# Performance work log

Hardware: AMD Instinct MI355X
Metric: run time of the kernel (lower is better)

Reference implementation:

```python
import jax, jax.numpy as jnp
import numpy as np

KV_POOL = 2


def setup_inputs() -> dict:
    key = jax.random.key(0)
    ks = jax.random.split(key, 12)
    B, C1, C2, H, W, D = 8, 256, 512, 64, 64, 64
    s = 0.02
    return {
        "x1": jax.random.normal(ks[0], (B, C1, H, W), jnp.float32),
        "x2": jax.random.normal(ks[1], (B, C2, H, W), jnp.float32),
        "Wq": jax.random.normal(ks[2], (D, C1), jnp.float32) * s,
        "bq": jnp.zeros((D,), jnp.float32),
        "Wk": jax.random.normal(ks[3], (D, C2), jnp.float32) * s,
        "bk": jnp.zeros((D,), jnp.float32),
        "Wv": jax.random.normal(ks[4], (D, C2), jnp.float32) * s,
        "bv": jnp.zeros((D,), jnp.float32),
        "Wo": jax.random.normal(ks[5], (C1, D), jnp.float32) * s,
        "bo": jnp.zeros((C1,), jnp.float32),
    }


def reference(x1, x2, Wq, bq, Wk, bk, Wv, bv, Wo, bo):
    B, C1, H, W = x1.shape
    D = Wq.shape[0]
    # adaptive_avg_pool2d to (H//2, W//2) with even dims == 2x2 mean pool
    Bs, C2, H2, W2 = x2.shape
    x2p = x2.reshape(Bs, C2, H2 // KV_POOL, KV_POOL, W2 // KV_POOL, KV_POOL).mean(axis=(3, 5))
    # 1x1 convs as channel matmuls; flatten spatial dims
    Q = jnp.einsum('bchw,dc->bhwd', x1, Wq).reshape(B, H * W, D) + bq          # [B,N,D]
    K = jnp.einsum('bchw,dc->bhwd', x2p, Wk).reshape(B, -1, D) + bk            # [B,M,D]
    V = jnp.einsum('bchw,dc->bhwd', x2p, Wv).reshape(B, -1, D) + bv            # [B,M,D]
    attn = jax.nn.softmax(jnp.einsum('bnd,bmd->bnm', Q, K), axis=-1)           # [B,N,M]
    out = jnp.einsum('bnm,bmd->bnd', attn, V)                                  # [B,N,D]
    y = jnp.einsum('bnd,cd->bnc', out, Wo) + bo                                # [B,N,C1]
    y = y.reshape(B, H, W, C1).transpose(0, 3, 1, 2)                           # [B,C1,H,W]
    return x1 + y
```

## Files before the change

### kernel.cpp

```cpp
#include <hip/hip_runtime.h>
#include <hip/hip_bf16.h>

typedef __bf16 bf16x4 __attribute__((ext_vector_type(4)));
typedef __bf16 bf16x8 __attribute__((ext_vector_type(8)));
typedef float f32x16 __attribute__((ext_vector_type(16)));
typedef unsigned int u32x4 __attribute__((ext_vector_type(4)));

static constexpr int Bc = 8, C1 = 256, C2 = 512, Hh = 64, Ww = 64, Dd = 64;
static constexpr int Nn = 4096, Mm = 1024;

#define MFMA __builtin_amdgcn_mfma_f32_32x32x16_bf16

__device__ __forceinline__ uint32_t pkbf(float a, float b) {
  union { __bf16 h[2]; uint32_t u; } x;
  x.h[0] = (__bf16)a; x.h[1] = (__bf16)b;
  return x.u;
}

__device__ __forceinline__ bf16x8 cvt8(const float* __restrict__ p) {
  float4 a = *(const float4*)p;
  float4 b2 = *(const float4*)(p + 4);
  bf16x8 r;
  r[0] = (__bf16)a.x; r[1] = (__bf16)a.y; r[2] = (__bf16)a.z; r[3] = (__bf16)a.w;
  r[4] = (__bf16)b2.x; r[5] = (__bf16)b2.y; r[6] = (__bf16)b2.z; r[7] = (__bf16)b2.w;
  return r;
}

__device__ __forceinline__ void pack16(const float* p, bf16x8& f0, bf16x8& f1) {
  uint32_t w01 = pkbf(p[0], p[1]),   w23 = pkbf(p[2], p[3]);
  uint32_t w45 = pkbf(p[4], p[5]),   w67 = pkbf(p[6], p[7]);
  uint32_t w89 = pkbf(p[8], p[9]),   wab = pkbf(p[10], p[11]);
  uint32_t wcd = pkbf(p[12], p[13]), wef = pkbf(p[14], p[15]);
  auto s0 = __builtin_amdgcn_permlane32_swap(w01, w45, false, false);
  auto s1 = __builtin_amdgcn_permlane32_swap(w23, w67, false, false);
  auto s2 = __builtin_amdgcn_permlane32_swap(w89, wcd, false, false);
  auto s3 = __builtin_amdgcn_permlane32_swap(wab, wef, false, false);
  u32x4 q0 = {s0[0], s1[0], s0[1], s1[1]};
  u32x4 q1 = {s2[0], s3[0], s2[1], s3[1]};
  f0 = __builtin_bit_cast(bf16x8, q0);
  f1 = __builtin_bit_cast(bf16x8, q1);
}


__global__ __launch_bounds__(256) void k_stage(
    const float* __restrict__ x1, const float* __restrict__ x2,
    const float* __restrict__ Wq, const float* __restrict__ Wk,
    const float* __restrict__ Wv, const float* __restrict__ Wo,
    __bf16* __restrict__ wqf, __bf16* __restrict__ wkf,
    __bf16* __restrict__ wvf, __bf16* __restrict__ wof,
    __bf16* __restrict__ x1f, __bf16* __restrict__ x2pf) {
  __shared__ __align__(16) __bf16 lds[32 * 132];
  const int lin = blockIdx.x, tid = threadIdx.x;
  if (lin >= 4096) {
    int t = (lin - 4096) * 256 + tid;
    if (t < 2048) {
      int l = t & 63, g = t >> 6, dh = g >> 4, ks = g & 15;
      int d = dh * 32 + (l & 31), c = ks * 16 + (l >> 5) * 8;
      *(bf16x8*)(wqf + (size_t)t * 8) = cvt8(Wq + (size_t)d * C1 + c);
    } else if (t < 6144) {
      int tt = t - 2048;
      int l = tt & 63, g = tt >> 6, dh = g >> 5, ks = g & 31;
      int d = dh * 32 + (l & 31), c = ks * 16 + (l >> 5) * 8;
      *(bf16x8*)(wkf + (size_t)tt * 8) = cvt8(Wk + (size_t)d * C2 + c);
    } else if (t < 10240) {
      int tt = t - 6144;
      int l = tt & 63, g = tt >> 6, dh = g >> 5, ks = g & 31;
      int d = dh * 32 + (l & 31), c = ks * 16 + (l >> 5) * 8;
      *(bf16x8*)(wvf + (size_t)tt * 8) = cvt8(Wv + (size_t)d * C2 + c);
    } else if (t < 12288) {
      int tt = t - 10240;
      int l = tt & 63, g = tt >> 6, ct = g >> 2, ks = g & 3;
      int crow = ct * 32 + (l & 31), d = ks * 16 + (l >> 5) * 8;
      *(bf16x8*)(wof + (size_t)tt * 8) = cvt8(Wo + (size_t)crow * Dd + d);
    }
    return;
  }
  const int b = lin & 7, idx = lin >> 3;
  const int w = tid >> 6, l = tid & 63;

  if (idx < 256) {
    const int t = idx >> 1, cc = idx & 1;
    const int n0 = t * 32, c0 = cc * 128;
#pragma unroll
    for (int it = 0; it < 4; ++it) {
      int cl = it * 32 + (tid >> 3);
      int q = tid & 7;
      float4 v = *(const float4*)(x1 + (size_t)(b * C1 + c0 + cl) * Nn + n0 + 4 * q);
      lds[(4 * q + 0) * 132 + cl] = (__bf16)v.x;
      lds[(4 * q + 1) * 132 + cl] = (__bf16)v.y;
      lds[(4 * q + 2) * 132 + cl] = (__bf16)v.z;
      lds[(4 * q + 3) * 132 + cl] = (__bf16)v.w;
    }
    __syncthreads();
#pragma unroll
    for (int j = 0; j < 2; ++j) {
      int ks8 = w * 2 + j;
      int off = (l & 31) * 132 + ks8 * 16 + (l >> 5) * 8;
      bf16x4 lo = *(const bf16x4*)(lds + off);
      bf16x4 hi = *(const bf16x4*)(lds + off + 4);
      __bf16* dst = x1f + ((size_t)(b * 128 + t) * 16 + cc * 8 + ks8) * 512 + l * 8;
      *(bf16x4*)dst = lo;
      *(bf16x4*)(dst + 4) = hi;
    }
  } else {
    const int idx2 = idx - 256;
    const int t = idx2 >> 3, cc = idx2 & 7;
    const int c0 = cc * 64;
    const int g = tid >> 4, lane16 = tid & 15, row = g & 1;
#pragma unroll
    for (int it = 0; it < 8; ++it) {
      int cl = it * 8 + (g >> 1);
      const float* p =
          x2 + ((size_t)(b * C2 + c0 + cl) * Hh + 2 * t + row) * Ww + 4 * lane16;
      float4 v = *(const float4*)p;
      float s0 = v.x + v.y, s1 = v.z + v.w;
      float p0 = (s0 + __shfl_xor(s0, 16)) * 0.25f;
      float p1 = (s1 + __shfl_xor(s1, 16)) * 0.25f;
      if (row == 0) {
        lds[(2 * lane16) * 68 + cl] = (__bf16)p0;
        lds[(2 * lane16 + 1) * 68 + cl] = (__bf16)p1;
      }
    }
    __syncthreads();
    const int ks8 = w;
    int off = (l & 31) * 68 + ks8 * 16 + (l >> 5) * 8;
    bf16x4 lo = *(const bf16x4*)(lds + off);
    bf16x4 hi = *(const bf16x4*)(lds + off + 4);
    __bf16* dst = x2pf + ((size_t)(b * 32 + t) * 32 + cc * 4 + ks8) * 512 + l * 8;
    *(bf16x4*)dst = lo;
    *(bf16x4*)(dst + 4) = hi;
  }
}

__global__ __launch_bounds__(256) void k_proj(
    const __bf16* __restrict__ x1f, const __bf16* __restrict__ x2pf,
    const __bf16* __restrict__ wqf, const float* __restrict__ bq,
    const __bf16* __restrict__ wkf, const float* __restrict__ bk,
    const __bf16* __restrict__ wvf, const float* __restrict__ bv,
    __bf16* __restrict__ qfb, __bf16* __restrict__ kfb,
    __bf16* __restrict__ vfb) {
  const int lin = blockIdx.x;
  const int b = lin & 7, idx = lin >> 3;
  const int tid = threadIdx.x;
  const int w = tid >> 6, l = tid & 63, h = l >> 5, nl = l & 31;

  if (idx < 64) {
    const int nsub = w & 1, dh = w >> 1;
    const int t = idx * 2 + nsub;
    const __bf16* af = x1f + ((size_t)(b * 128 + t) * 16) * 512 + l * 8;
    const __bf16* wf = wqf + (size_t)dh * 16 * 512 + l * 8;
    f32x16 acc = {};
#pragma unroll
    for (int ks = 0; ks < 16; ++ks) {
      bf16x8 a = *(const bf16x8*)(af + ks * 512);
      bf16x8 bb = *(const bf16x8*)(wf + ks * 512);
      acc = MFMA(a, bb, acc, 0, 0, 0);
    }
    const int d = dh * 32 + nl;
    const float bias = bq[d];
    __bf16* qdst = qfb + (size_t)b * Nn * Dd + (size_t)t * 2048 +
                   (d >> 4) * 512 + ((d >> 3) & 1) * 256 + (d & 7);
#pragma unroll
    for (int r = 0; r < 16; ++r) {
      int mrow = (r & 3) + 8 * (r >> 2) + 4 * h;
      qdst[mrow * 8] = (__bf16)(acc[r] + bias);
    }
  } else {
    const int h2 = idx - 64;
    const int isv = w >> 1, dh = w & 1;
    const __bf16* af = x2pf + ((size_t)(b * 32 + h2) * 32) * 512 + l * 8;
    const __bf16* wf = (isv ? wvf : wkf) + (size_t)dh * 32 * 512 + l * 8;
    f32x16 acc = {};
#pragma unroll
    for (int ks = 0; ks < 32; ++ks) {
      bf16x8 a = *(const bf16x8*)(af + ks * 512);
      bf16x8 bb = *(const bf16x8*)(wf + ks * 512);
      acc = MFMA(a, bb, acc, 0, 0, 0);
    }
    const int d = dh * 32 + nl;
    if (!isv) {
      const float bias = bk[d];
      __bf16* kdst = kfb + (size_t)b * Mm * Dd + (size_t)h2 * 2048 +
                     (d >> 4) * 512 + ((d >> 3) & 1) * 256 + (d & 7);
#pragma unroll
      for (int r = 0; r < 16; ++r) {
        int mr = (r & 3) + 8 * (r >> 2) + 4 * h;
        kdst[mr * 8] = (__bf16)(acc[r] + bias);
      }
    } else {
      const float bias = bv[d];
      float ov[16];
#pragma unroll
      for (int r = 0; r < 16; ++r) ov[r] = acc[r] + bias;
      bf16x8 f0, f1;
      pack16(ov, f0, f1);
      __bf16* vdst = vfb + (size_t)b * Mm * Dd + (size_t)h2 * 2048 + l * 8;
      *(bf16x8*)(vdst + (size_t)dh * 512) = f0;
      *(bf16x8*)(vdst + (size_t)(2 + dh) * 512) = f1;
    }
  }
}

template <int S>
__global__ __launch_bounds__(256) void k_attn_part(
    const __bf16* __restrict__ qfb, const __bf16* __restrict__ kfb,
    const __bf16* __restrict__ vfb, __bf16* __restrict__ po,
    float* __restrict__ pml) {
  const int lin = blockIdx.x;
  const int b = lin & 7, rest = lin >> 3, nblk = rest & 31, sp = rest >> 5;
  const int tid = threadIdx.x;
  const int w = tid >> 6, l = tid & 63, h = l >> 5, nl = l & 31;
  const int n = nblk * 128 + w * 32 + nl;
  constexpr int NT = Mm / S / 32;
  const int t0 = sp * NT;

  const __bf16* qt = qfb + (size_t)b * Nn * Dd + (size_t)(nblk * 4 + w) * 2048 + l * 8;
  bf16x8 qf0 = *(const bf16x8*)(qt);
  bf16x8 qf1 = *(const bf16x8*)(qt + 512);
  bf16x8 qf2 = *(const bf16x8*)(qt + 1024);
  bf16x8 qf3 = *(const bf16x8*)(qt + 1536);

  const __bf16* kt = kfb + (size_t)b * Mm * Dd + (size_t)t0 * 2048 + l * 8;
  const __bf16* vt = vfb + (size_t)b * Mm * Dd + (size_t)t0 * 2048 + l * 8;

  f32x16 o0 = {}, o1 = {};
  float lsum = 0.f;

  bf16x8 ck0 = *(const bf16x8*)(kt);
  bf16x8 ck1 = *(const bf16x8*)(kt + 512);
  bf16x8 ck2 = *(const bf16x8*)(kt + 1024);
  bf16x8 ck3 = *(const bf16x8*)(kt + 1536);
  bf16x8 cv0 = *(const bf16x8*)(vt);
  bf16x8 cv1 = *(const bf16x8*)(vt + 512);
  bf16x8 cv2 = *(const bf16x8*)(vt + 1024);
  bf16x8 cv3 = *(const bf16x8*)(vt + 1536);

#pragma unroll
  for (int i = 0; i < NT; ++i) {
    bf16x8 nk0, nk1, nk2, nk3, nv0, nv1, nv2, nv3;
    if (i + 1 < NT) {
      const __bf16* kn = kt + (size_t)(i + 1) * 2048;
      const __bf16* vn = vt + (size_t)(i + 1) * 2048;
      nk0 = *(const bf16x8*)(kn);
      nk1 = *(const bf16x8*)(kn + 512);
      nk2 = *(const bf16x8*)(kn + 1024);
      nk3 = *(const bf16x8*)(kn + 1536);
      nv0 = *(const bf16x8*)(vn);
      nv1 = *(const bf16x8*)(vn + 512);
      nv2 = *(const bf16x8*)(vn + 1024);
      nv3 = *(const bf16x8*)(vn + 1536);
    }
    f32x16 s = {};
    s = MFMA(ck0, qf0, s, 0, 0, 0);
    s = MFMA(ck1, qf1, s, 0, 0, 0);
    s = MFMA(ck2, qf2, s, 0, 0, 0);
    s = MFMA(ck3, qf3, s, 0, 0, 0);
    float p[16];
#pragma unroll
    for (int r = 0; r < 16; ++r) p[r] = __expf(s[r]);
    float u0 = (p[0] + p[1]) + (p[2] + p[3]);
    float u1 = (p[4] + p[5]) + (p[6] + p[7]);
    float u2 = (p[8] + p[9]) + (p[10] + p[11]);
    float u3 = (p[12] + p[13]) + (p[14] + p[15]);
    lsum += (u0 + u1) + (u2 + u3);
    bf16x8 pb0, pb1;
    pack16(p, pb0, pb1);
    o0 = MFMA(cv0, pb0, o0, 0, 0, 0);
    o1 = MFMA(cv1, pb0, o1, 0, 0, 0);
    o0 = MFMA(cv2, pb1, o0, 0, 0, 0);
    o1 = MFMA(cv3, pb1, o1, 0, 0, 0);
    if (i + 1 < NT) {
      ck0 = nk0; ck1 = nk1; ck2 = nk2; ck3 = nk3;
      cv0 = nv0; cv1 = nv1; cv2 = nv2; cv3 = nv3;
    }
  }

  const float ltot = lsum + __shfl_xor(lsum, 32);
  __bf16* ob = po + (size_t)(b * S + sp) * 16 * Nn * 4 + (size_t)n * 4;
#pragma unroll
  for (int q = 0; q < 4; ++q) {
    bf16x4 t0v, t1v;
#pragma unroll
    for (int e = 0; e < 4; ++e) {
      t0v[e] = (__bf16)o0[q * 4 + e];
      t1v[e] = (__bf16)o1[q * 4 + e];
    }
    *(bf16x4*)(ob + (size_t)(2 * q + h) * Nn * 4) = t0v;
    *(bf16x4*)(ob + (size_t)(8 + 2 * q + h) * Nn * 4) = t1v;
  }
  if (h == 0) pml[(size_t)(b * S + sp) * Nn + n] = ltot;
}

template <int S>
__global__ __launch_bounds__(256) void k_attn_comb(
    const float* __restrict__ x1, const __bf16* __restrict__ po,
    const float* __restrict__ pml, const __bf16* __restrict__ wof,
    const float* __restrict__ bo, float* __restrict__ out) {
  const int lin = blockIdx.x;
  const int b = lin & 7, rest = lin >> 3, nblk = rest & 31, ctg = rest >> 5;
  const int tid = threadIdx.x;
  const int w = tid >> 6, l = tid & 63, h = l >> 5, nl = l & 31;
  const int n = nblk * 128 + w * 32 + nl;

  float L = 0.f;
#pragma unroll
  for (int s = 0; s < S; ++s)
    L += pml[(size_t)(b * S + s) * Nn + n];
  const float inv = 1.f / L;

  float o[32];
#pragma unroll
  for (int r = 0; r < 32; ++r) o[r] = 0.f;
#pragma unroll
  for (int s = 0; s < S; ++s) {
    const __bf16* ob = po + (size_t)(b * S + s) * 16 * Nn * 4 + (size_t)n * 4;
#pragma unroll
    for (int q = 0; q < 4; ++q) {
      bf16x4 v0 = *(const bf16x4*)(ob + (size_t)(2 * q + h) * Nn * 4);
      bf16x4 v1 = *(const bf16x4*)(ob + (size_t)(8 + 2 * q + h) * Nn * 4);
#pragma unroll
      for (int e = 0; e < 4; ++e) {
        o[q * 4 + e] += (float)v0[e];
        o[16 + q * 4 + e] += (float)v1[e];
      }
    }
  }

  bf16x8 obf[4];
#pragma unroll
  for (int a2 = 0; a2 < 2; ++a2) {
    float ov[16];
#pragma unroll
    for (int r = 0; r < 16; ++r) ov[r] = o[a2 * 16 + r] * inv;
    pack16(ov, obf[a2 * 2], obf[a2 * 2 + 1]);
  }

  const float* x1r = x1 + (size_t)b * C1 * Nn + n;
  float* outr = out + (size_t)b * C1 * Nn + n;
#pragma unroll
  for (int ci = 0; ci < 4; ++ci) {
    const int ct = ctg * 4 + ci;
    f32x16 y = {};
#pragma unroll
    for (int ks = 0; ks < 4; ++ks) {
      bf16x8 a = *(const bf16x8*)(wof + (size_t)((ct * 4 + ks) * 64 + l) * 8);
      y = MFMA(a, obf[ks], y, 0, 0, 0);
    }
#pragma unroll
    for (int r = 0; r < 16; ++r) {
      int c = ct * 32 + (r & 3) + 8 * (r >> 2) + 4 * h;
      size_t idx = (size_t)c * Nn;
      outr[idx] = y[r] + bo[c] + x1r[idx];
    }
  }
}

__global__ __launch_bounds__(256) void k_attn(
    const float* __restrict__ x1, const __bf16* __restrict__ qfb,
    const __bf16* __restrict__ kfb, const __bf16* __restrict__ vfb,
    const __bf16* __restrict__ wof, const float* __restrict__ bo,
    float* __restrict__ out) {
  const int b = blockIdx.y, tid = threadIdx.x;
  const int w = tid >> 6, l = tid & 63, h = l >> 5, nl = l & 31;
  const int n = blockIdx.x * 128 + w * 32 + nl;

  const __bf16* qt = qfb + (size_t)b * Nn * Dd + (size_t)(blockIdx.x * 4 + w) * 2048 + l * 8;
  bf16x8 qf0 = *(const bf16x8*)(qt);
  bf16x8 qf1 = *(const bf16x8*)(qt + 512);
  bf16x8 qf2 = *(const bf16x8*)(qt + 1024);
  bf16x8 qf3 = *(const bf16x8*)(qt + 1536);

  f32x16 o0 = {}, o1 = {};
  float mrun = -INFINITY, lsum = 0.f;

  const __bf16* kb_ = kfb + (size_t)b * Mm * Dd + l * 8;
  const __bf16* vb_ = vfb + (size_t)b * Mm * Dd + l * 8;

  for (int t = 0; t < 32; ++t) {
    const __bf16* kt = kb_ + (size_t)t * 2048;
    const __bf16* vt = vb_ + (size_t)t * 2048;
    bf16x8 ka0 = *(const bf16x8*)(kt);
    bf16x8 ka1 = *(const bf16x8*)(kt + 512);
    bf16x8 ka2 = *(const bf16x8*)(kt + 1024);
    bf16x8 ka3 = *(const bf16x8*)(kt + 1536);
    bf16x8 v00 = *(const bf16x8*)(vt);
    bf16x8 v10 = *(const bf16x8*)(vt + 512);
    bf16x8 v01 = *(const bf16x8*)(vt + 1024);
    bf16x8 v11 = *(const bf16x8*)(vt + 1536);
    f32x16 s = {};
    s = MFMA(ka0, qf0, s, 0, 0, 0);
    s = MFMA(ka1, qf1, s, 0, 0, 0);
    s = MFMA(ka2, qf2, s, 0, 0, 0);
    s = MFMA(ka3, qf3, s, 0, 0, 0);
    float tmax = s[0];
#pragma unroll
    for (int r = 1; r < 16; ++r) tmax = fmaxf(tmax, s[r]);
    tmax = fmaxf(tmax, __shfl_xor(tmax, 32));
    const float mnew = fmaxf(mrun, tmax);
    const float scale = __expf(mrun - mnew);
    float p[16], psum = 0.f;
#pragma unroll
    for (int r = 0; r < 16; ++r) { p[r] = __expf(s[r] - mnew); psum += p[r]; }
    lsum = lsum * scale + psum;
    mrun = mnew;
#pragma unroll
    for (int r = 0; r < 16; ++r) { o0[r] *= scale; o1[r] *= scale; }
    bf16x8 pb0, pb1;
    pack16(p, pb0, pb1);
    o0 = MFMA(v00, pb0, o0, 0, 0, 0);
    o1 = MFMA(v10, pb0, o1, 0, 0, 0);
    o0 = MFMA(v01, pb1, o0, 0, 0, 0);
    o1 = MFMA(v11, pb1, o1, 0, 0, 0);
  }

  const float ltot = lsum + __shfl_xor(lsum, 32);
  const float inv = 1.f / ltot;

  bf16x8 ob[4];
#pragma unroll
  for (int a2 = 0; a2 < 2; ++a2) {
    float ov[16];
#pragma unroll
    for (int r = 0; r < 16; ++r) ov[r] = (a2 ? o1[r] : o0[r]) * inv;
    pack16(ov, ob[a2 * 2], ob[a2 * 2 + 1]);
  }

  const float* x1r = x1 + (size_t)b * C1 * Nn + n;
  float* outr = out + (size_t)b * C1 * Nn + n;
#pragma unroll 2
  for (int ct = 0; ct < 8; ++ct) {
    f32x16 y = {};
#pragma unroll
    for (int ks = 0; ks < 4; ++ks) {
      bf16x8 a = *(const bf16x8*)(wof + (size_t)((ct * 4 + ks) * 64 + l) * 8);
      y = MFMA(a, ob[ks], y, 0, 0, 0);
    }
#pragma unroll
    for (int r = 0; r < 16; ++r) {
      int c = ct * 32 + (r & 3) + 8 * (r >> 2) + 4 * h;
      size_t idx = (size_t)c * Nn;
      outr[idx] = y[r] + bo[c] + x1r[idx];
    }
  }
}

extern "C" void kernel_launch(void* const* d_in, const int* in_sizes, int n_in,
                              void* d_out, int out_size, void* d_ws,
                              size_t ws_size, hipStream_t stream) {
  const float* x1 = (const float*)d_in[0];
  const float* x2 = (const float*)d_in[1];
  const float* Wq = (const float*)d_in[2];
  const float* bq = (const float*)d_in[3];
  const float* Wk = (const float*)d_in[4];
  const float* bk = (const float*)d_in[5];
  const float* Wv = (const float*)d_in[6];
  const float* bv = (const float*)d_in[7];
  const float* Wo = (const float*)d_in[8];
  const float* bo = (const float*)d_in[9];
  float* out = (float*)d_out;
  char* ws = (char*)d_ws;

  __bf16* wqf  = (__bf16*)(ws);
  __bf16* wkf  = (__bf16*)(ws + 32768);
  __bf16* wvf  = (__bf16*)(ws + 98304);
  __bf16* wof  = (__bf16*)(ws + 163840);
  __bf16* qfb  = (__bf16*)(ws + 196608);
  __bf16* kfb  = (__bf16*)(ws + 4390912);
  __bf16* vfb  = (__bf16*)(ws + 5439488);
  __bf16* x1f  = (__bf16*)(ws + 6488064);
  __bf16* x2pf = (__bf16*)(ws + 23265280);
  __bf16* po   = (__bf16*)(ws + 31653888);
  const size_t ws8 = 31653888ull + 33554432ull + 1048576ull;
  const size_t ws4 = 31653888ull + 16777216ull + 524288ull;

  hipLaunchKernelGGL(k_stage, dim3(4144), dim3(256), 0, stream,
                     x1, x2, Wq, Wk, Wv, Wo, wqf, wkf, wvf, wof, x1f, x2pf);
  hipLaunchKernelGGL(k_proj, dim3(768), dim3(256), 0, stream,
                     x1f, x2pf, wqf, bq, wkf, bk, wvf, bv, qfb, kfb, vfb);
  if (ws_size >= ws8) {
    float* pml = (float*)(ws + 31653888 + 33554432);
    hipLaunchKernelGGL(k_attn_part<8>, dim3(32 * 8 * 8), dim3(256), 0, stream,
                       qfb, kfb, vfb, po, pml);
    hipLaunchKernelGGL(k_attn_comb<8>, dim3(32 * 8 * 2), dim3(256), 0, stream,
                       x1, po, pml, wof, bo, out);
  } else if (ws_size >= ws4) {
    float* pml = (float*)(ws + 31653888 + 16777216);
    hipLaunchKernelGGL(k_attn_part<4>, dim3(32 * 8 * 4), dim3(256), 0, stream,
                       qfb, kfb, vfb, po, pml);
    hipLaunchKernelGGL(k_attn_comb<4>, dim3(32 * 8 * 2), dim3(256), 0, stream,
                       x1, po, pml, wof, bo, out);
  } else {
    hipLaunchKernelGGL(k_attn, dim3(32, 8), dim3(256), 0, stream,
                       x1, qfb, kfb, vfb, wof, bo, out);
  }
}
```

Before: 66.45 us.

## Restructure staging kernel into larger tiles with contiguous row reads and fewer blocks

The staging kernel that converts x1 to bf16 fragment layout and pools x2 is reorganized so each block handles a 16-channel by 512-position tile, reading whole contiguous spatial rows per channel. The block count drops accordingly, and LDS is reshaped to channel-major with a transposed gather on write-out. The aim is more coalesced, longer global reads and less per-block overhead for this bandwidth-bound preprocessing. In exchange, LDS reads become scalar strided gathers that may cause bank conflicts, and fewer blocks means less parallelism.

After: 65.03 us. 2.1% less time.

```diff
diff --git a/kernel.cpp b/kernel.cpp
--- a/kernel.cpp
+++ b/kernel.cpp
@@ -1,6 +1,7 @@
 #include <hip/hip_runtime.h>
 #include <hip/hip_bf16.h>
 
+typedef __bf16 bf16x2 __attribute__((ext_vector_type(2)));
 typedef __bf16 bf16x4 __attribute__((ext_vector_type(4)));
 typedef __bf16 bf16x8 __attribute__((ext_vector_type(8)));
 typedef float f32x16 __attribute__((ext_vector_type(16)));
@@ -49,86 +50,97 @@
     __bf16* __restrict__ wqf, __bf16* __restrict__ wkf,
     __bf16* __restrict__ wvf, __bf16* __restrict__ wof,
     __bf16* __restrict__ x1f, __bf16* __restrict__ x2pf) {
-  __shared__ __align__(16) __bf16 lds[32 * 132];
+  __shared__ __align__(16) __bf16 lds[16 * 516];
   const int lin = blockIdx.x, tid = threadIdx.x;
-  if (lin >= 4096) {
-    int t = (lin - 4096) * 256 + tid;
+  const int w = tid >> 6, l = tid & 63;
+
+  if (lin >= 1280) {
+    int t = (lin - 1280) * 256 + tid;
     if (t < 2048) {
-      int l = t & 63, g = t >> 6, dh = g >> 4, ks = g & 15;
-      int d = dh * 32 + (l & 31), c = ks * 16 + (l >> 5) * 8;
+      int ll = t & 63, g = t >> 6, dh = g >> 4, ks = g & 15;
+      int d = dh * 32 + (ll & 31), c = ks * 16 + (ll >> 5) * 8;
       *(bf16x8*)(wqf + (size_t)t * 8) = cvt8(Wq + (size_t)d * C1 + c);
     } else if (t < 6144) {
       int tt = t - 2048;
-      int l = tt & 63, g = tt >> 6, dh = g >> 5, ks = g & 31;
-      int d = dh * 32 + (l & 31), c = ks * 16 + (l >> 5) * 8;
+      int ll = tt & 63, g = tt >> 6, dh = g >> 5, ks = g & 31;
+      int d = dh * 32 + (ll & 31), c = ks * 16 + (ll >> 5) * 8;
       *(bf16x8*)(wkf + (size_t)tt * 8) = cvt8(Wk + (size_t)d * C2 + c);
     } else if (t < 10240) {
       int tt = t - 6144;
-      int l = tt & 63, g = tt >> 6, dh = g >> 5, ks = g & 31;
-      int d = dh * 32 + (l & 31), c = ks * 16 + (l >> 5) * 8;
+      int ll = tt & 63, g = tt >> 6, dh = g >> 5, ks = g & 31;
+      int d = dh * 32 + (ll & 31), c = ks * 16 + (ll >> 5) * 8;
       *(bf16x8*)(wvf + (size_t)tt * 8) = cvt8(Wv + (size_t)d * C2 + c);
     } else if (t < 12288) {
       int tt = t - 10240;
-      int l = tt & 63, g = tt >> 6, ct = g >> 2, ks = g & 3;
-      int crow = ct * 32 + (l & 31), d = ks * 16 + (l >> 5) * 8;
+      int ll = tt & 63, g = tt >> 6, ct = g >> 2, ks = g & 3;
+      int crow = ct * 32 + (ll & 31), d = ks * 16 + (ll >> 5) * 8;
       *(bf16x8*)(wof + (size_t)tt * 8) = cvt8(Wo + (size_t)crow * Dd + d);
     }
     return;
   }
-  const int b = lin & 7, idx = lin >> 3;
-  const int w = tid >> 6, l = tid & 63;
-
-  if (idx < 256) {
-    const int t = idx >> 1, cc = idx & 1;
-    const int n0 = t * 32, c0 = cc * 128;
-#pragma unroll
-    for (int it = 0; it < 4; ++it) {
-      int cl = it * 32 + (tid >> 3);
-      int q = tid & 7;
-      float4 v = *(const float4*)(x1 + (size_t)(b * C1 + c0 + cl) * Nn + n0 + 4 * q);
-      lds[(4 * q + 0) * 132 + cl] = (__bf16)v.x;
-      lds[(4 * q + 1) * 132 + cl] = (__bf16)v.y;
-      lds[(4 * q + 2) * 132 + cl] = (__bf16)v.z;
-      lds[(4 * q + 3) * 132 + cl] = (__bf16)v.w;
+
+  if (lin < 256) {
+    const int b = lin & 7, q = lin >> 3;
+    const int ks2 = q & 15, half = q >> 4;
+#pragma unroll
+    for (int cc = 0; cc < 4; ++cc) {
+      const int c_loc = w * 4 + cc;
+      const int c = ks2 * 16 + c_loc;
+      const float* src = x2 + ((size_t)(b * C2 + c) * Hh + half * 32) * Ww;
+#pragma unroll
+      for (int it = 0; it < 8; ++it) {
+        float4 v = *(const float4*)(src + it * 256 + l * 4);
+        float s0 = v.x + v.y, s1 = v.z + v.w;
+        float p0 = (s0 + __shfl_xor(s0, 16)) * 0.25f;
+        float p1 = (s1 + __shfl_xor(s1, 16)) * 0.25f;
+        const int rl = l >> 4;
+        if ((rl & 1) == 0) {
+          int h2l = it * 2 + (rl >> 1);
+          bf16x2 pv; pv[0] = (__bf16)p0; pv[1] = (__bf16)p1;
+          *(bf16x2*)(lds + c_loc * 516 + h2l * 32 + 2 * (l & 15)) = pv;
+        }
+      }
     }
     __syncthreads();
 #pragma unroll
-    for (int j = 0; j < 2; ++j) {
-      int ks8 = w * 2 + j;
-      int off = (l & 31) * 132 + ks8 * 16 + (l >> 5) * 8;
-      bf16x4 lo = *(const bf16x4*)(lds + off);
-      bf16x4 hi = *(const bf16x4*)(lds + off + 4);
-      __bf16* dst = x1f + ((size_t)(b * 128 + t) * 16 + cc * 8 + ks8) * 512 + l * 8;
-      *(bf16x4*)dst = lo;
-      *(bf16x4*)(dst + 4) = hi;
+    for (int ti = 0; ti < 4; ++ti) {
+      const int t_loc = w * 4 + ti;
+      bf16x8 f;
+#pragma unroll
+      for (int e = 0; e < 8; ++e)
+        f[e] = lds[((l >> 5) * 8 + e) * 516 + t_loc * 32 + (l & 31)];
+      const int t_m = half * 16 + t_loc;
+      *(bf16x8*)(x2pf + ((size_t)(b * 32 + t_m) * 32 + ks2) * 512 + l * 8) = f;
     }
   } else {
-    const int idx2 = idx - 256;
-    const int t = idx2 >> 3, cc = idx2 & 7;
-    const int c0 = cc * 64;
-    const int g = tid >> 4, lane16 = tid & 15, row = g & 1;
-#pragma unroll
-    for (int it = 0; it < 8; ++it) {
-      int cl = it * 8 + (g >> 1);
-      const float* p =
-          x2 + ((size_t)(b * C2 + c0 + cl) * Hh + 2 * t + row) * Ww + 4 * lane16;
-      float4 v = *(const float4*)p;
-      float s0 = v.x + v.y, s1 = v.z + v.w;
-      float p0 = (s0 + __shfl_xor(s0, 16)) * 0.25f;
-      float p1 = (s1 + __shfl_xor(s1, 16)) * 0.25f;
-      if (row == 0) {
-        lds[(2 * lane16) * 68 + cl] = (__bf16)p0;
-        lds[(2 * lane16 + 1) * 68 + cl] = (__bf16)p1;
+    const int e0 = lin - 256;
+    const int b = e0 & 7, r = e0 >> 3;
+    const int ks = r & 15, nch = r >> 4;
+    const int n0 = nch * 512;
+#pragma unroll
+    for (int cc = 0; cc < 4; ++cc) {
+      const int c_loc = w * 4 + cc;
+      const float* src = x1 + (size_t)(b * C1 + ks * 16 + c_loc) * Nn + n0;
+#pragma unroll
+      for (int j = 0; j < 2; ++j) {
+        float4 v = *(const float4*)(src + j * 256 + l * 4);
+        bf16x4 t4;
+        t4[0] = (__bf16)v.x; t4[1] = (__bf16)v.y;
+        t4[2] = (__bf16)v.z; t4[3] = (__bf16)v.w;
+        *(bf16x4*)(lds + c_loc * 516 + j * 256 + l * 4) = t4;
       }
     }
     __syncthreads();
-    const int ks8 = w;
-    int off = (l & 31) * 68 + ks8 * 16 + (l >> 5) * 8;
-    bf16x4 lo = *(const bf16x4*)(lds + off);
-    bf16x4 hi = *(const bf16x4*)(lds + off + 4);
-    __bf16* dst = x2pf + ((size_t)(b * 32 + t) * 32 + cc * 4 + ks8) * 512 + l * 8;
-    *(bf16x4*)dst = lo;
-    *(bf16x4*)(dst + 4) = hi;
+#pragma unroll
+    for (int ti = 0; ti < 4; ++ti) {
+      const int t_loc = w * 4 + ti;
+      bf16x8 f;
+#pragma unroll
+      for (int e = 0; e < 8; ++e)
+        f[e] = lds[((l >> 5) * 8 + e) * 516 + t_loc * 32 + (l & 31)];
+      const int t = nch * 16 + t_loc;
+      *(bf16x8*)(x1f + ((size_t)(b * 128 + t) * 16 + ks) * 512 + l * 8) = f;
+    }
   }
 }
 
@@ -473,7 +485,7 @@
   const size_t ws8 = 31653888ull + 33554432ull + 1048576ull;
   const size_t ws4 = 31653888ull + 16777216ull + 524288ull;
 
-  hipLaunchKernelGGL(k_stage, dim3(4144), dim3(256), 0, stream,
+  hipLaunchKernelGGL(k_stage, dim3(1328), dim3(256), 0, stream,
                      x1, x2, Wq, Wk, Wv, Wo, wqf, wkf, wvf, wof, x1f, x2pf);
   hipLaunchKernelGGL(k_proj, dim3(768), dim3(256), 0, stream,
                      x1f, x2pf, wqf, bq, wkf, bk, wvf, bv, qfb, kfb, vfb);
```

## Split split-K combine into separate reduction kernel and output GEMM

Applied to the files above, without the earlier changes.

The fused combine kernel, which both reduced the split partial attention outputs and ran the Wo projection, is split in two. A lightweight elementwise reduction kernel first writes normalized bf16 combined outputs to a new workspace buffer. A separate GEMM kernel then reads them and runs over twice as many blocks, each handling half the output channel tiles. This removes the redundant re-reduction of partials across channel-group blocks and raises parallelism, at the cost of an extra launch, a larger workspace requirement, and an extra write and read of the intermediate.

After: 75.16 us. +13.1%, slower.

```diff
diff --git a/kernel.cpp b/kernel.cpp
--- a/kernel.cpp
+++ b/kernel.cpp
@@ -1,6 +1,7 @@
 #include <hip/hip_runtime.h>
 #include <hip/hip_bf16.h>
 
+typedef __bf16 bf16x2 __attribute__((ext_vector_type(2)));
 typedef __bf16 bf16x4 __attribute__((ext_vector_type(4)));
 typedef __bf16 bf16x8 __attribute__((ext_vector_type(8)));
 typedef float f32x16 __attribute__((ext_vector_type(16)));
@@ -292,54 +293,60 @@
 }
 
 template <int S>
-__global__ __launch_bounds__(256) void k_attn_comb(
-    const float* __restrict__ x1, const __bf16* __restrict__ po,
-    const float* __restrict__ pml, const __bf16* __restrict__ wof,
-    const float* __restrict__ bo, float* __restrict__ out) {
+__global__ __launch_bounds__(256) void k_red(
+    const __bf16* __restrict__ po, const float* __restrict__ pml,
+    __bf16* __restrict__ cmb) {
+  const int g = blockIdx.x * 256 + threadIdx.x;
+  const int n = g & (Nn - 1);
+  const int dgrp = (g >> 12) & 15;
+  const int b = g >> 16;
+  float L = 0.f;
+#pragma unroll
+  for (int s = 0; s < S; ++s) L += pml[(size_t)(b * S + s) * Nn + n];
+  const float inv = 1.f / L;
+  float a0 = 0.f, a1 = 0.f, a2 = 0.f, a3 = 0.f;
+#pragma unroll
+  for (int s = 0; s < S; ++s) {
+    bf16x4 v = *(const bf16x4*)(po + ((size_t)((b * S + s) * 16 + dgrp) * Nn + n) * 4);
+    a0 += (float)v[0]; a1 += (float)v[1]; a2 += (float)v[2]; a3 += (float)v[3];
+  }
+  bf16x4 o;
+  o[0] = (__bf16)(a0 * inv); o[1] = (__bf16)(a1 * inv);
+  o[2] = (__bf16)(a2 * inv); o[3] = (__bf16)(a3 * inv);
+  *(bf16x4*)(cmb + ((size_t)(b * 16 + dgrp) * Nn + n) * 4) = o;
+}
+
+__global__ __launch_bounds__(256) void k_cgemm(
+    const float* __restrict__ x1, const __bf16* __restrict__ cmb,
+    const __bf16* __restrict__ wof, const float* __restrict__ bo,
+    float* __restrict__ out) {
   const int lin = blockIdx.x;
   const int b = lin & 7, rest = lin >> 3, nblk = rest & 31, ctg = rest >> 5;
   const int tid = threadIdx.x;
   const int w = tid >> 6, l = tid & 63, h = l >> 5, nl = l & 31;
   const int n = nblk * 128 + w * 32 + nl;
 
-  float L = 0.f;
-#pragma unroll
-  for (int s = 0; s < S; ++s)
-    L += pml[(size_t)(b * S + s) * Nn + n];
-  const float inv = 1.f / L;
-
   float o[32];
 #pragma unroll
-  for (int r = 0; r < 32; ++r) o[r] = 0.f;
-#pragma unroll
-  for (int s = 0; s < S; ++s) {
-    const __bf16* ob = po + (size_t)(b * S + s) * 16 * Nn * 4 + (size_t)n * 4;
-#pragma unroll
-    for (int q = 0; q < 4; ++q) {
-      bf16x4 v0 = *(const bf16x4*)(ob + (size_t)(2 * q + h) * Nn * 4);
-      bf16x4 v1 = *(const bf16x4*)(ob + (size_t)(8 + 2 * q + h) * Nn * 4);
-#pragma unroll
-      for (int e = 0; e < 4; ++e) {
-        o[q * 4 + e] += (float)v0[e];
-        o[16 + q * 4 + e] += (float)v1[e];
-      }
+  for (int q = 0; q < 4; ++q) {
+    bf16x4 v0 = *(const bf16x4*)(cmb + ((size_t)(b * 16 + 2 * q + h) * Nn + n) * 4);
+    bf16x4 v1 = *(const bf16x4*)(cmb + ((size_t)(b * 16 + 8 + 2 * q + h) * Nn + n) * 4);
+#pragma unroll
+    for (int e = 0; e < 4; ++e) {
+      o[q * 4 + e] = (float)v0[e];
+      o[16 + q * 4 + e] = (float)v1[e];
     }
   }
 
   bf16x8 obf[4];
-#pragma unroll
-  for (int a2 = 0; a2 < 2; ++a2) {
-    float ov[16];
-#pragma unroll
-    for (int r = 0; r < 16; ++r) ov[r] = o[a2 * 16 + r] * inv;
-    pack16(ov, obf[a2 * 2], obf[a2 * 2 + 1]);
-  }
+  pack16(o, obf[0], obf[1]);
+  pack16(o + 16, obf[2], obf[3]);
 
   const float* x1r = x1 + (size_t)b * C1 * Nn + n;
   float* outr = out + (size_t)b * C1 * Nn + n;
 #pragma unroll
-  for (int ci = 0; ci < 4; ++ci) {
-    const int ct = ctg * 4 + ci;
+  for (int ci = 0; ci < 2; ++ci) {
+    const int ct = ctg * 2 + ci;
     f32x16 y = {};
 #pragma unroll
     for (int ks = 0; ks < 4; ++ks) {
@@ -470,25 +477,30 @@
   __bf16* x1f  = (__bf16*)(ws + 6488064);
   __bf16* x2pf = (__bf16*)(ws + 23265280);
   __bf16* po   = (__bf16*)(ws + 31653888);
-  const size_t ws8 = 31653888ull + 33554432ull + 1048576ull;
-  const size_t ws4 = 31653888ull + 16777216ull + 524288ull;
+  const size_t po_off = 31653888ull;
+  const size_t ws8 = po_off + 33554432ull + 1048576ull + 4194304ull;
+  const size_t ws4 = po_off + 16777216ull + 524288ull + 4194304ull;
 
   hipLaunchKernelGGL(k_stage, dim3(4144), dim3(256), 0, stream,
                      x1, x2, Wq, Wk, Wv, Wo, wqf, wkf, wvf, wof, x1f, x2pf);
   hipLaunchKernelGGL(k_proj, dim3(768), dim3(256), 0, stream,
                      x1f, x2pf, wqf, bq, wkf, bk, wvf, bv, qfb, kfb, vfb);
   if (ws_size >= ws8) {
-    float* pml = (float*)(ws + 31653888 + 33554432);
+    float*  pml = (float*)(ws + po_off + 33554432ull);
+    __bf16* cmb = (__bf16*)(ws + po_off + 33554432ull + 1048576ull);
     hipLaunchKernelGGL(k_attn_part<8>, dim3(32 * 8 * 8), dim3(256), 0, stream,
                        qfb, kfb, vfb, po, pml);
-    hipLaunchKernelGGL(k_attn_comb<8>, dim3(32 * 8 * 2), dim3(256), 0, stream,
-                       x1, po, pml, wof, bo, out);
+    hipLaunchKernelGGL(k_red<8>, dim3(2048), dim3(256), 0, stream, po, pml, cmb);
+    hipLaunchKernelGGL(k_cgemm, dim3(32 * 8 * 4), dim3(256), 0, stream,
+                       x1, cmb, wof, bo, out);
   } else if (ws_size >= ws4) {
-    float* pml = (float*)(ws + 31653888 + 16777216);
+    float*  pml = (float*)(ws + po_off + 16777216ull);
+    __bf16* cmb = (__bf16*)(ws + po_off + 16777216ull + 524288ull);
     hipLaunchKernelGGL(k_attn_part<4>, dim3(32 * 8 * 4), dim3(256), 0, stream,
                        qfb, kfb, vfb, po, pml);
-    hipLaunchKernelGGL(k_attn_comb<4>, dim3(32 * 8 * 2), dim3(256), 0, stream,
-                       x1, po, pml, wof, bo, out);
+    hipLaunchKernelGGL(k_red<4>, dim3(2048), dim3(256), 0, stream, po, pml, cmb);
+    hipLaunchKernelGGL(k_cgemm, dim3(32 * 8 * 4), dim3(256), 0, stream,
+                       x1, cmb, wof, bo, out);
   } else {
     hipLaunchKernelGGL(k_attn, dim3(32, 8), dim3(256), 0, stream,
                        x1, qfb, kfb, vfb, wof, bo, out);
```
